# Performance work log

Measured on AMD Instinct MI355X. Metric: run time of the kernel, lower is better.

## Reference

```python
import jax, jax.numpy as jnp
import numpy as np

B, S, D = 1, 4096, 1024
H, W = 16, 512            # heads, window_size
HD = D // H               # head_dim = 64


def setup_inputs() -> dict:
    key = jax.random.key(0)
    k1, k2, k3 = jax.random.split(key, 3)
    x = jax.random.normal(k1, (B, S, D), dtype=jnp.float32)
    w_qkv = jax.random.normal(k2, (D, 3 * D), dtype=jnp.float32) * 0.02
    w_out = jax.random.normal(k3, (D, D), dtype=jnp.float32) * 0.02
    return {"x": x, "w_qkv": w_qkv, "w_out": w_out}


def reference(x, w_qkv, w_out):
    b, s, d = x.shape
    qkv = x @ w_qkv                                   # [B,S,3D]
    q, k, v = jnp.split(qkv, 3, axis=-1)
    to_heads = lambda t: t.reshape(b, s, H, HD).transpose(0, 2, 1, 3)  # [B,H,S,hd]
    q, k, v = map(to_heads, (q, k, v))

    C = s // W                                        # number of chunks
    qc = q.reshape(b, H, C, W, HD)                    # [B,H,C,W,hd]
    kc = k.reshape(b, H, C, W, HD)
    vc = v.reshape(b, H, C, W, HD)

    # each chunk attends to [previous chunk, current chunk] of K/V (2W keys)
    zero = jnp.zeros_like(kc[:, :, :1])
    k_prev = jnp.concatenate([zero, kc[:, :, :-1]], axis=2)
    v_prev = jnp.concatenate([jnp.zeros_like(vc[:, :, :1]), vc[:, :, :-1]], axis=2)
    kcat = jnp.concatenate([k_prev, kc], axis=3)      # [B,H,C,2W,hd]
    vcat = jnp.concatenate([v_prev, vc], axis=3)

    scores = jnp.einsum('bhcqd,bhckd->bhcqk', qc, kcat) / (HD ** 0.5)

    # mask: causal (abs q_pos >= abs k_pos) and k_pos >= 0 (first chunk has no prev)
    wq = jnp.arange(W)
    jk = jnp.arange(2 * W)
    ci = jnp.arange(C)
    causal = (wq[:, None] + W) >= jk[None, :]                    # [W,2W]
    valid = (ci[:, None, None] * W + jk[None, None, :] - W) >= 0  # [C,1,2W]
    mask = causal[None] & valid                                   # [C,W,2W]

    scores = jnp.where(mask[None, None], scores, -jnp.inf)
    attn = jax.nn.softmax(scores, axis=-1)
    out = jnp.einsum('bhcqk,bhckd->bhcqd', attn, vcat)            # [B,H,C,W,hd]
    out = out.reshape(b, H, s, HD).transpose(0, 2, 1, 3).reshape(b, s, d)
    return out @ w_out
```

## Files before the change

### kernel.cpp

```cpp
#include <hip/hip_runtime.h>

typedef __attribute__((ext_vector_type(8))) short short8;
typedef __attribute__((ext_vector_type(4))) float f32x4;
typedef unsigned short u16;

__device__ __forceinline__ u16 f2bf(float f) {
  unsigned int u = __float_as_uint(f);
  u += 0x7fffu + ((u >> 16) & 1u);
  return (u16)(u >> 16);
}

__device__ __forceinline__ void gld16(const void* g, void* l) {
  __builtin_amdgcn_global_load_lds((const __attribute__((address_space(1))) void*)g,
                                   (__attribute__((address_space(3))) void*)l, 16, 0, 0);
}

__global__ __launch_bounds__(256) void cast_f32_to_bf16(const float* __restrict__ in,
                                                        u16* __restrict__ out, int n8) {
  int i = blockIdx.x * 256 + threadIdx.x;
  if (i >= n8) return;
  const f32x4* p = (const f32x4*)in;
  f32x4 a = p[i * 2];
  f32x4 b = p[i * 2 + 1];
  short8 o;
#pragma unroll
  for (int j = 0; j < 4; ++j) o[j] = (short)f2bf(a[j]);
#pragma unroll
  for (int j = 0; j < 4; ++j) o[4 + j] = (short)f2bf(b[j]);
  ((short8*)out)[i] = o;
}

__global__ __launch_bounds__(256) void transpose_cast(const float* __restrict__ w,
                                                      u16* __restrict__ wT, int K, int N) {
  __shared__ float tile[32][33];
  int n0 = blockIdx.x * 32, k0 = blockIdx.y * 32;
  int r = threadIdx.x >> 5;
  int c = threadIdx.x & 31;
#pragma unroll
  for (int i = 0; i < 4; ++i)
    tile[r + i * 8][c] = w[(size_t)(k0 + r + i * 8) * N + n0 + c];
  __syncthreads();
#pragma unroll
  for (int i = 0; i < 4; ++i)
    wT[(size_t)(n0 + r + i * 8) * K + k0 + c] = f2bf(tile[c][r + i * 8]);
}

template <int MODE>
__global__ __launch_bounds__(256) void gemm_bf16(
    const u16* __restrict__ A, const u16* __restrict__ Bt, float* __restrict__ C,
    u16* __restrict__ q_out, u16* __restrict__ k_out, u16* __restrict__ v_out,
    int M, int N, int K) {
  __shared__ __align__(16) u16 As[128][64];
  __shared__ __align__(16) u16 Bs[128][64];
  const int t = threadIdx.x;
  const int lane = t & 63;
  const int wid = t >> 6;
  const int wm = wid >> 1, wn = wid & 1;
  const int l15 = lane & 15, lhi = lane >> 4;

  const int nbx = gridDim.x;
  const int bid = blockIdx.y * nbx + blockIdx.x;
  const int cpx = (nbx * gridDim.y) >> 3;
  const int wg = (bid & 7) * cpx + (bid >> 3);
  const int m0 = (wg / nbx) * 128;
  const int n0 = (wg % nbx) * 128;

  const int srow = lane >> 3;
  const int scol = (lane & 7) * 8;

  f32x4 acc[4][4];
#pragma unroll
  for (int mi = 0; mi < 4; ++mi)
#pragma unroll
    for (int ni = 0; ni < 4; ++ni) acc[mi][ni] = (f32x4){0.f, 0.f, 0.f, 0.f};

  for (int k0 = 0; k0 < K; k0 += 64) {
    __syncthreads();
#pragma unroll
    for (int i = 0; i < 4; ++i) {
      int cch = wid * 4 + i;
      int row = cch * 8 + srow;
      gld16(&A[(size_t)(m0 + row) * K + k0 + scol], &As[cch * 8][0]);
      gld16(&Bt[(size_t)(n0 + row) * K + k0 + scol], &Bs[cch * 8][0]);
    }
    __syncthreads();
#pragma unroll
    for (int kc = 0; kc < 2; ++kc) {
      short8 af[4], bf[4];
#pragma unroll
      for (int mi = 0; mi < 4; ++mi)
        af[mi] = *(const short8*)&As[wm * 64 + mi * 16 + l15][kc * 32 + lhi * 8];
#pragma unroll
      for (int ni = 0; ni < 4; ++ni)
        bf[ni] = *(const short8*)&Bs[wn * 64 + ni * 16 + l15][kc * 32 + lhi * 8];
#pragma unroll
      for (int mi = 0; mi < 4; ++mi)
#pragma unroll
        for (int ni = 0; ni < 4; ++ni)
          acc[mi][ni] = __builtin_amdgcn_mfma_f32_16x16x32_bf16(af[mi], bf[ni], acc[mi][ni], 0, 0, 0);
    }
  }

#pragma unroll
  for (int mi = 0; mi < 4; ++mi)
#pragma unroll
    for (int ni = 0; ni < 4; ++ni)
#pragma unroll
      for (int r = 0; r < 4; ++r) {
        int row = m0 + wm * 64 + mi * 16 + lhi * 4 + r;
        int col = n0 + wn * 64 + ni * 16 + l15;
        float val = acc[mi][ni][r];
        if (MODE == 0) {
          C[(size_t)row * N + col] = val;
        } else {
          int which = col >> 10;
          int d = col & 1023;
          int hh = d >> 6, hd = d & 63;
          u16* dst = (which == 0) ? q_out : ((which == 1) ? k_out : v_out);
          dst[((size_t)hh * 4096 + row) * 64 + hd] = f2bf(val);
        }
      }
}

__global__ __launch_bounds__(256) void attn_kernel(
    const u16* __restrict__ qh,
    const u16* __restrict__ kh,
    const u16* __restrict__ vh,
    u16* __restrict__ out) {
  __shared__ __align__(16) u16 Ks[2][64][64];
  __shared__ __align__(16) u16 Vt[2][66][64];
  __shared__ __align__(16) u16 Pl[4][32][72];

  const int t = threadIdx.x;
  const int lane = t & 63;
  const int w = t >> 6;
  const int l15 = lane & 15;
  const int lhi = lane >> 4;

  const int bid = blockIdx.x;
  const int wk = (bid & 7) * 64 + (bid >> 3);
  const int qt = wk & 3, c = (wk >> 2) & 7, h = wk >> 5;

  const long head_base = (long)h * 4096 * 64;
  const int q0 = qt * 128;
  const long q_gbase = head_base + (long)(c * 512 + q0) * 64;

  short8 qf[2][2];
#pragma unroll
  for (int mi = 0; mi < 2; ++mi)
#pragma unroll
    for (int kc = 0; kc < 2; ++kc)
      qf[mi][kc] = *(const short8*)&qh[q_gbase + (long)(w * 32 + mi * 16 + l15) * 64 + kc * 32 + lhi * 8];

  if (t < 128) Vt[t >> 6][64][t & 63] = 0x3F80;

  float m_run[8];
  f32x4 acc_o[2][4], acc_l[2];
#pragma unroll
  for (int i = 0; i < 8; ++i) m_run[i] = -1e30f;
#pragma unroll
  for (int mi = 0; mi < 2; ++mi) {
    acc_l[mi] = (f32x4){0.f, 0.f, 0.f, 0.f};
#pragma unroll
    for (int ni = 0; ni < 4; ++ni) acc_o[mi][ni] = (f32x4){0.f, 0.f, 0.f, 0.f};
  }

  const int kt_start = (c == 0) ? 8 : 0;
  const int kt_end = 2 * qt + 9;
  const long kv_base = head_base + ((long)c - 1) * 512 * 64;

  const int ksrow = lane >> 3;
  const int kscol = ((lane & 7) ^ (lane >> 3)) * 8;
  const int vr = t >> 3, vg = t & 7;

  {
    const int j0 = kt_start * 64;
#pragma unroll
    for (int i = 0; i < 2; ++i) {
      int cch = w * 2 + i;
      gld16(&kh[kv_base + (long)(j0 + cch * 8 + ksrow) * 64 + kscol], &Ks[0][cch * 8][0]);
    }
#pragma unroll
    for (int i = 0; i < 2; ++i) {
      int r = vr + i * 32;
      short8 vv = *(const short8*)&vh[kv_base + (long)(j0 + r) * 64 + vg * 8];
#pragma unroll
      for (int j = 0; j < 8; ++j) Vt[0][vg * 8 + j][r ^ ((vg ^ j) << 3)] = (u16)vv[j];
    }
  }
  __syncthreads();

  int cur = 0;
  for (int kt = kt_start; kt <= kt_end; ++kt) {
    const int j0 = kt * 64;
    const int nxt = cur ^ 1;
    const bool has_next = (kt < kt_end);

    short8 vpre[2];
    if (has_next) {
      const int j0n = j0 + 64;
#pragma unroll
      for (int i = 0; i < 2; ++i) {
        int cch = w * 2 + i;
        gld16(&kh[kv_base + (long)(j0n + cch * 8 + ksrow) * 64 + kscol], &Ks[nxt][cch * 8][0]);
      }
#pragma unroll
      for (int i = 0; i < 2; ++i)
        vpre[i] = *(const short8*)&vh[kv_base + (long)(j0n + vr + i * 32) * 64 + vg * 8];
    }

    const bool active = (j0 <= q0 + w * 32 + 31 + 512);
    if (active) {
      f32x4 sa[2][4];
#pragma unroll
      for (int mi = 0; mi < 2; ++mi)
#pragma unroll
        for (int ni = 0; ni < 4; ++ni) sa[mi][ni] = (f32x4){0.f, 0.f, 0.f, 0.f};
#pragma unroll
      for (int kc = 0; kc < 2; ++kc) {
        short8 kf[4];
#pragma unroll
        for (int ni = 0; ni < 4; ++ni) {
          int row = ni * 16 + l15;
          int colu = (kc * 4 + lhi) ^ (row & 7);
          kf[ni] = *(const short8*)&Ks[cur][row][colu * 8];
        }
#pragma unroll
        for (int mi = 0; mi < 2; ++mi)
#pragma unroll
          for (int ni = 0; ni < 4; ++ni)
            sa[mi][ni] = __builtin_amdgcn_mfma_f32_16x16x32_bf16(qf[mi][kc], kf[ni], sa[mi][ni], 0, 0, 0);
      }

      const float SC = 0.18033688011112042f;
      const int qrow0 = q0 + w * 32 + lhi * 4;
      const bool need_mask = (j0 + 63 > q0 + w * 32 + 512);
      float tmax[8];
#pragma unroll
      for (int i = 0; i < 8; ++i) tmax[i] = -1e30f;
      if (need_mask) {
#pragma unroll
        for (int mi = 0; mi < 2; ++mi)
#pragma unroll
          for (int ni = 0; ni < 4; ++ni) {
            int jj = j0 + ni * 16 + l15;
#pragma unroll
            for (int r = 0; r < 4; ++r) {
              float sv = sa[mi][ni][r] * SC;
              sv = (qrow0 + mi * 16 + r + 512 >= jj) ? sv : -1e30f;
              sa[mi][ni][r] = sv;
              tmax[mi * 4 + r] = fmaxf(tmax[mi * 4 + r], sv);
            }
          }
      } else {
#pragma unroll
        for (int mi = 0; mi < 2; ++mi)
#pragma unroll
          for (int ni = 0; ni < 4; ++ni)
#pragma unroll
            for (int r = 0; r < 4; ++r) {
              float sv = sa[mi][ni][r] * SC;
              sa[mi][ni][r] = sv;
              tmax[mi * 4 + r] = fmaxf(tmax[mi * 4 + r], sv);
            }
      }
#pragma unroll
      for (int i = 0; i < 8; ++i)
#pragma unroll
        for (int d = 1; d < 16; d <<= 1)
          tmax[i] = fmaxf(tmax[i], __shfl_xor(tmax[i], d, 64));

      float corr[8];
#pragma unroll
      for (int i = 0; i < 8; ++i) {
        float mn = fmaxf(m_run[i], tmax[i]);
        corr[i] = __builtin_amdgcn_exp2f(m_run[i] - mn);
        m_run[i] = mn;
      }
#pragma unroll
      for (int mi = 0; mi < 2; ++mi)
#pragma unroll
        for (int ni = 0; ni < 4; ++ni)
#pragma unroll
          for (int r = 0; r < 4; ++r) {
            float p = __builtin_amdgcn_exp2f(sa[mi][ni][r] - m_run[mi * 4 + r]);
            Pl[w][mi * 16 + lhi * 4 + r][ni * 16 + l15] = f2bf(p);
          }
#pragma unroll
      for (int mi = 0; mi < 2; ++mi) {
#pragma unroll
        for (int r = 0; r < 4; ++r) acc_l[mi][r] *= corr[mi * 4 + r];
#pragma unroll
        for (int ni = 0; ni < 4; ++ni)
#pragma unroll
          for (int r = 0; r < 4; ++r) acc_o[mi][ni][r] *= corr[mi * 4 + r];
      }
    }

    if (has_next) {
#pragma unroll
      for (int i = 0; i < 2; ++i) {
        int r = vr + i * 32;
#pragma unroll
        for (int j = 0; j < 8; ++j) Vt[nxt][vg * 8 + j][r ^ ((vg ^ j) << 3)] = (u16)vpre[i][j];
      }
    }

    if (active) {
#pragma unroll
      for (int k2 = 0; k2 < 2; ++k2) {
        short8 pf[2];
#pragma unroll
        for (int mi = 0; mi < 2; ++mi)
          pf[mi] = *(const short8*)&Pl[w][mi * 16 + l15][k2 * 32 + lhi * 8];
        short8 vones = *(const short8*)&Vt[cur][64][k2 * 32 + lhi * 8];
#pragma unroll
        for (int mi = 0; mi < 2; ++mi)
          acc_l[mi] = __builtin_amdgcn_mfma_f32_16x16x32_bf16(pf[mi], vones, acc_l[mi], 0, 0, 0);
#pragma unroll
        for (int ni = 0; ni < 4; ++ni) {
          int row = ni * 16 + l15;
          int S = ((row >> 3) ^ row) & 7;
          short8 vf = *(const short8*)&Vt[cur][row][(k2 * 32 + lhi * 8) ^ (S << 3)];
#pragma unroll
          for (int mi = 0; mi < 2; ++mi)
            acc_o[mi][ni] = __builtin_amdgcn_mfma_f32_16x16x32_bf16(pf[mi], vf, acc_o[mi][ni], 0, 0, 0);
        }
      }
    }
    __syncthreads();
    cur = nxt;
  }

#pragma unroll
  for (int mi = 0; mi < 2; ++mi)
#pragma unroll
    for (int ni = 0; ni < 4; ++ni)
#pragma unroll
      for (int r = 0; r < 4; ++r) {
        int qq = q0 + w * 32 + mi * 16 + lhi * 4 + r;
        long s = (long)c * 512 + qq;
        int col = h * 64 + ni * 16 + l15;
        float o = acc_o[mi][ni][r] / acc_l[mi][r];
        out[s * 1024 + col] = f2bf(o);
      }
}

extern "C" void kernel_launch(void* const* d_in, const int* in_sizes, int n_in,
                              void* d_out, int out_size, void* d_ws, size_t ws_size,
                              hipStream_t stream) {
  const float* x = (const float*)d_in[0];
  const float* w_qkv = (const float*)d_in[1];
  const float* w_out = (const float*)d_in[2];
  float* out = (float*)d_out;

  u16* xb = (u16*)d_ws;
  u16* wqkvT = xb + 4096 * 1024;
  u16* woutT = wqkvT + 3072 * 1024;
  u16* qh = woutT + 1024 * 1024;
  u16* kh = qh + 16 * 4096 * 64;
  u16* vh = kh + 16 * 4096 * 64;
  u16* attn = xb;

  cast_f32_to_bf16<<<2048, 256, 0, stream>>>(x, xb, 4096 * 1024 / 8);
  transpose_cast<<<dim3(96, 32), 256, 0, stream>>>(w_qkv, wqkvT, 1024, 3072);
  transpose_cast<<<dim3(32, 32), 256, 0, stream>>>(w_out, woutT, 1024, 1024);

  gemm_bf16<1><<<dim3(24, 32), 256, 0, stream>>>(xb, wqkvT, nullptr, qh, kh, vh,
                                                 4096, 3072, 1024);
  attn_kernel<<<512, 256, 0, stream>>>(qh, kh, vh, attn);
  gemm_bf16<0><<<dim3(8, 32), 256, 0, stream>>>(attn, woutT, out, nullptr, nullptr, nullptr,
                                                4096, 1024, 1024);
}
```

Baseline: 213.7 us.

## Halve attention query tile per block and add MFMA priority hints

The attention kernel now handles 64 query rows per block, 16 per wave, instead of 128 rows, which doubles the grid to 1024 blocks and cuts per-thread accumulator registers. The aim is more parallelism and occupancy across the CUs, plus less causal-tail imbalance between blocks. Each K/V tile is now loaded from global memory and staged in LDS by twice as many blocks, which raises memory traffic and makes each MFMA load do less work. s_setprio is also raised around the MFMA sections so that wave's matrix work is scheduled ahead of other waves.

```diff
diff --git a/kernel.cpp b/kernel.cpp
--- a/kernel.cpp
+++ b/kernel.cpp
@@ -129,7 +129,7 @@
     u16* __restrict__ out) {
   __shared__ __align__(16) u16 Ks[2][64][64];
   __shared__ __align__(16) u16 Vt[2][66][64];
-  __shared__ __align__(16) u16 Pl[4][32][72];
+  __shared__ __align__(16) u16 Pl[4][16][72];
 
   const int t = threadIdx.x;
   const int lane = t & 63;
@@ -138,35 +138,30 @@
   const int lhi = lane >> 4;
 
   const int bid = blockIdx.x;
-  const int wk = (bid & 7) * 64 + (bid >> 3);
-  const int qt = wk & 3, c = (wk >> 2) & 7, h = wk >> 5;
+  const int wk = (bid & 7) * 128 + (bid >> 3);
+  const int qt = wk & 7, c = (wk >> 3) & 7, h = wk >> 6;
 
   const long head_base = (long)h * 4096 * 64;
-  const int q0 = qt * 128;
+  const int q0 = qt * 64;
   const long q_gbase = head_base + (long)(c * 512 + q0) * 64;
 
-  short8 qf[2][2];
-#pragma unroll
-  for (int mi = 0; mi < 2; ++mi)
-#pragma unroll
-    for (int kc = 0; kc < 2; ++kc)
-      qf[mi][kc] = *(const short8*)&qh[q_gbase + (long)(w * 32 + mi * 16 + l15) * 64 + kc * 32 + lhi * 8];
+  short8 qf[2];
+#pragma unroll
+  for (int kc = 0; kc < 2; ++kc)
+    qf[kc] = *(const short8*)&qh[q_gbase + (long)(w * 16 + l15) * 64 + kc * 32 + lhi * 8];
 
   if (t < 128) Vt[t >> 6][64][t & 63] = 0x3F80;
 
-  float m_run[8];
-  f32x4 acc_o[2][4], acc_l[2];
-#pragma unroll
-  for (int i = 0; i < 8; ++i) m_run[i] = -1e30f;
-#pragma unroll
-  for (int mi = 0; mi < 2; ++mi) {
-    acc_l[mi] = (f32x4){0.f, 0.f, 0.f, 0.f};
-#pragma unroll
-    for (int ni = 0; ni < 4; ++ni) acc_o[mi][ni] = (f32x4){0.f, 0.f, 0.f, 0.f};
-  }
+  float m_run[4];
+  f32x4 acc_o[4], acc_l;
+#pragma unroll
+  for (int i = 0; i < 4; ++i) m_run[i] = -1e30f;
+  acc_l = (f32x4){0.f, 0.f, 0.f, 0.f};
+#pragma unroll
+  for (int ni = 0; ni < 4; ++ni) acc_o[ni] = (f32x4){0.f, 0.f, 0.f, 0.f};
 
   const int kt_start = (c == 0) ? 8 : 0;
-  const int kt_end = 2 * qt + 9;
+  const int kt_end = qt + 8;
   const long kv_base = head_base + ((long)c - 1) * 512 * 64;
 
   const int ksrow = lane >> 3;
@@ -209,13 +204,12 @@
         vpre[i] = *(const short8*)&vh[kv_base + (long)(j0n + vr + i * 32) * 64 + vg * 8];
     }
 
-    const bool active = (j0 <= q0 + w * 32 + 31 + 512);
+    const bool active = (j0 <= q0 + w * 16 + 15 + 512);
     if (active) {
-      f32x4 sa[2][4];
-#pragma unroll
-      for (int mi = 0; mi < 2; ++mi)
-#pragma unroll
-        for (int ni = 0; ni < 4; ++ni) sa[mi][ni] = (f32x4){0.f, 0.f, 0.f, 0.f};
+      f32x4 sa[4];
+#pragma unroll
+      for (int ni = 0; ni < 4; ++ni) sa[ni] = (f32x4){0.f, 0.f, 0.f, 0.f};
+      __builtin_amdgcn_s_setprio(1);
 #pragma unroll
       for (int kc = 0; kc < 2; ++kc) {
         short8 kf[4];
@@ -226,75 +220,65 @@
           kf[ni] = *(const short8*)&Ks[cur][row][colu * 8];
         }
 #pragma unroll
-        for (int mi = 0; mi < 2; ++mi)
-#pragma unroll
-          for (int ni = 0; ni < 4; ++ni)
-            sa[mi][ni] = __builtin_amdgcn_mfma_f32_16x16x32_bf16(qf[mi][kc], kf[ni], sa[mi][ni], 0, 0, 0);
-      }
+        for (int ni = 0; ni < 4; ++ni)
+          sa[ni] = __builtin_amdgcn_mfma_f32_16x16x32_bf16(qf[kc], kf[ni], sa[ni], 0, 0, 0);
+      }
+      __builtin_amdgcn_s_setprio(0);
 
       const float SC = 0.18033688011112042f;
-      const int qrow0 = q0 + w * 32 + lhi * 4;
-      const bool need_mask = (j0 + 63 > q0 + w * 32 + 512);
-      float tmax[8];
-#pragma unroll
-      for (int i = 0; i < 8; ++i) tmax[i] = -1e30f;
+      const int qrow0 = q0 + w * 16 + lhi * 4;
+      const bool need_mask = (j0 + 63 > q0 + w * 16 + 512);
+      float tmax[4];
+#pragma unroll
+      for (int i = 0; i < 4; ++i) tmax[i] = -1e30f;
       if (need_mask) {
 #pragma unroll
-        for (int mi = 0; mi < 2; ++mi)
-#pragma unroll
-          for (int ni = 0; ni < 4; ++ni) {
-            int jj = j0 + ni * 16 + l15;
-#pragma unroll
-            for (int r = 0; r < 4; ++r) {
-              float sv = sa[mi][ni][r] * SC;
-              sv = (qrow0 + mi * 16 + r + 512 >= jj) ? sv : -1e30f;
-              sa[mi][ni][r] = sv;
-              tmax[mi * 4 + r] = fmaxf(tmax[mi * 4 + r], sv);
-            }
+        for (int ni = 0; ni < 4; ++ni) {
+          int jj = j0 + ni * 16 + l15;
+#pragma unroll
+          for (int r = 0; r < 4; ++r) {
+            float sv = sa[ni][r] * SC;
+            sv = (qrow0 + r + 512 >= jj) ? sv : -1e30f;
+            sa[ni][r] = sv;
+            tmax[r] = fmaxf(tmax[r], sv);
           }
+        }
       } else {
 #pragma unroll
-        for (int mi = 0; mi < 2; ++mi)
-#pragma unroll
-          for (int ni = 0; ni < 4; ++ni)
-#pragma unroll
-            for (int r = 0; r < 4; ++r) {
-              float sv = sa[mi][ni][r] * SC;
-              sa[mi][ni][r] = sv;
-              tmax[mi * 4 + r] = fmaxf(tmax[mi * 4 + r], sv);
-            }
-      }
-#pragma unroll
-      for (int i = 0; i < 8; ++i)
+        for (int ni = 0; ni < 4; ++ni)
+#pragma unroll
+          for (int r = 0; r < 4; ++r) {
+            float sv = sa[ni][r] * SC;
+            sa[ni][r] = sv;
+            tmax[r] = fmaxf(tmax[r], sv);
+          }
+      }
+#pragma unroll
+      for (int i = 0; i < 4; ++i)
 #pragma unroll
         for (int d = 1; d < 16; d <<= 1)
           tmax[i] = fmaxf(tmax[i], __shfl_xor(tmax[i], d, 64));
 
-      float corr[8];
-#pragma unroll
-      for (int i = 0; i < 8; ++i) {
+      float corr[4];
+#pragma unroll
+      for (int i = 0; i < 4; ++i) {
         float mn = fmaxf(m_run[i], tmax[i]);
         corr[i] = __builtin_amdgcn_exp2f(m_run[i] - mn);
         m_run[i] = mn;
       }
 #pragma unroll
-      for (int mi = 0; mi < 2; ++mi)
-#pragma unroll
-        for (int ni = 0; ni < 4; ++ni)
-#pragma unroll
-          for (int r = 0; r < 4; ++r) {
-            float p = __builtin_amdgcn_exp2f(sa[mi][ni][r] - m_run[mi * 4 + r]);
-            Pl[w][mi * 16 + lhi * 4 + r][ni * 16 + l15] = f2bf(p);
-          }
-#pragma unroll
-      for (int mi = 0; mi < 2; ++mi) {
-#pragma unroll
-        for (int r = 0; r < 4; ++r) acc_l[mi][r] *= corr[mi * 4 + r];
-#pragma unroll
-        for (int ni = 0; ni < 4; ++ni)
-#pragma unroll
-          for (int r = 0; r < 4; ++r) acc_o[mi][ni][r] *= corr[mi * 4 + r];
-      }
+      for (int ni = 0; ni < 4; ++ni)
+#pragma unroll
+        for (int r = 0; r < 4; ++r) {
+          float p = __builtin_amdgcn_exp2f(sa[ni][r] - m_run[r]);
+          Pl[w][lhi * 4 + r][ni * 16 + l15] = f2bf(p);
+        }
+#pragma unroll
+      for (int r = 0; r < 4; ++r) acc_l[r] *= corr[r];
+#pragma unroll
+      for (int ni = 0; ni < 4; ++ni)
+#pragma unroll
+        for (int r = 0; r < 4; ++r) acc_o[ni][r] *= corr[r];
     }
 
     if (has_next) {
@@ -307,43 +291,36 @@
     }
 
     if (active) {
+      __builtin_amdgcn_s_setprio(1);
 #pragma unroll
       for (int k2 = 0; k2 < 2; ++k2) {
-        short8 pf[2];
-#pragma unroll
-        for (int mi = 0; mi < 2; ++mi)
-          pf[mi] = *(const short8*)&Pl[w][mi * 16 + l15][k2 * 32 + lhi * 8];
+        short8 pf = *(const short8*)&Pl[w][l15][k2 * 32 + lhi * 8];
         short8 vones = *(const short8*)&Vt[cur][64][k2 * 32 + lhi * 8];
-#pragma unroll
-        for (int mi = 0; mi < 2; ++mi)
-          acc_l[mi] = __builtin_amdgcn_mfma_f32_16x16x32_bf16(pf[mi], vones, acc_l[mi], 0, 0, 0);
+        acc_l = __builtin_amdgcn_mfma_f32_16x16x32_bf16(pf, vones, acc_l, 0, 0, 0);
 #pragma unroll
         for (int ni = 0; ni < 4; ++ni) {
           int row = ni * 16 + l15;
           int S = ((row >> 3) ^ row) & 7;
           short8 vf = *(const short8*)&Vt[cur][row][(k2 * 32 + lhi * 8) ^ (S << 3)];
-#pragma unroll
-          for (int mi = 0; mi < 2; ++mi)
-            acc_o[mi][ni] = __builtin_amdgcn_mfma_f32_16x16x32_bf16(pf[mi], vf, acc_o[mi][ni], 0, 0, 0);
-        }
-      }
+          acc_o[ni] = __builtin_amdgcn_mfma_f32_16x16x32_bf16(pf, vf, acc_o[ni], 0, 0, 0);
+        }
+      }
+      __builtin_amdgcn_s_setprio(0);
     }
     __syncthreads();
     cur = nxt;
   }
 
 #pragma unroll
-  for (int mi = 0; mi < 2; ++mi)
-#pragma unroll
-    for (int ni = 0; ni < 4; ++ni)
-#pragma unroll
-      for (int r = 0; r < 4; ++r) {
-        int qq = q0 + w * 32 + mi * 16 + lhi * 4 + r;
-        long s = (long)c * 512 + qq;
-        int col = h * 64 + ni * 16 + l15;
-        float o = acc_o[mi][ni][r] / acc_l[mi][r];
-        out[s * 1024 + col] = f2bf(o);
-      }
+  for (int ni = 0; ni < 4; ++ni)
+#pragma unroll
+    for (int r = 0; r < 4; ++r) {
+      int qq = q0 + w * 16 + lhi * 4 + r;
+      long s = (long)c * 512 + qq;
+      int col = h * 64 + ni * 16 + l15;
+      float o = acc_o[ni][r] / acc_l[r];
+      out[s * 1024 + col] = f2bf(o);
+    }
 }
 
 extern "C" void kernel_launch(void* const* d_in, const int* in_sizes, int n_in,
@@ -368,7 +345,7 @@
 
   gemm_bf16<1><<<dim3(24, 32), 256, 0, stream>>>(xb, wqkvT, nullptr, qh, kh, vh,
                                                  4096, 3072, 1024);
-  attn_kernel<<<512, 256, 0, stream>>>(qh, kh, vh, attn);
+  attn_kernel<<<1024, 256, 0, stream>>>(qh, kh, vh, attn);
   gemm_bf16<0><<<dim3(8, 32), 256, 0, stream>>>(attn, woutT, out, nullptr, nullptr, nullptr,
                                                 4096, 1024, 1024);
 }
```

After: 219.0 us. +2.4%, slower.

## Pre-transpose V, head-major attention output, swizzled GEMM LDS, fold Q scale

Applied to the files above, without the earlier changes.

Adds a separate kernel that transposes V per head. The attention kernel can then fill its V tile with direct global-to-LDS loads instead of transposing through registers and doing scattered LDS stores. Attention output is written head-major in place over the Q buffer, and the output GEMM gains a mode that reads this layout, with a narrower N tile (BN=64) to launch more blocks. The GEMM's LDS tiles are now XOR-swizzled to cut bank conflicts. The softmax scale is folded into Q in the QKV GEMM epilogue, which removes a multiply per score in attention. The cost is one extra kernel launch and an extra pass over V in memory.

```diff
diff --git a/kernel.cpp b/kernel.cpp
--- a/kernel.cpp
+++ b/kernel.cpp
@@ -45,13 +45,30 @@
     wT[(size_t)(n0 + r + i * 8) * K + k0 + c] = f2bf(tile[c][r + i * 8]);
 }
 
-template <int MODE>
+__global__ __launch_bounds__(256) void transpose_v(const u16* __restrict__ vh,
+                                                   u16* __restrict__ vt) {
+  __shared__ u16 tile[32][33];
+  const int s0 = blockIdx.x * 32, d0 = blockIdx.y * 32, h = blockIdx.z;
+  const long hb = (long)h * 4096 * 64;
+  const long hb2 = (long)h * 64 * 4096;
+  const int r = threadIdx.x >> 5, c = threadIdx.x & 31;
+#pragma unroll
+  for (int i = 0; i < 4; ++i)
+    tile[r + i * 8][c] = vh[hb + (long)(s0 + r + i * 8) * 64 + d0 + c];
+  __syncthreads();
+#pragma unroll
+  for (int i = 0; i < 4; ++i)
+    vt[hb2 + (long)(d0 + r + i * 8) * 4096 + s0 + c] = tile[c][r + i * 8];
+}
+
+template <int MODE, int BN>
 __global__ __launch_bounds__(256) void gemm_bf16(
     const u16* __restrict__ A, const u16* __restrict__ Bt, float* __restrict__ C,
     u16* __restrict__ q_out, u16* __restrict__ k_out, u16* __restrict__ v_out,
     int M, int N, int K) {
   __shared__ __align__(16) u16 As[128][64];
-  __shared__ __align__(16) u16 Bs[128][64];
+  __shared__ __align__(16) u16 Bs[BN][64];
+  constexpr int NW = BN / 32;
   const int t = threadIdx.x;
   const int lane = t & 63;
   const int wid = t >> 6;
@@ -63,16 +80,16 @@
   const int cpx = (nbx * gridDim.y) >> 3;
   const int wg = (bid & 7) * cpx + (bid >> 3);
   const int m0 = (wg / nbx) * 128;
-  const int n0 = (wg % nbx) * 128;
+  const int n0 = (wg % nbx) * BN;
 
   const int srow = lane >> 3;
-  const int scol = (lane & 7) * 8;
-
-  f32x4 acc[4][4];
+  const int scol = ((lane & 7) ^ (lane >> 3)) * 8;
+
+  f32x4 acc[4][NW];
 #pragma unroll
   for (int mi = 0; mi < 4; ++mi)
 #pragma unroll
-    for (int ni = 0; ni < 4; ++ni) acc[mi][ni] = (f32x4){0.f, 0.f, 0.f, 0.f};
+    for (int ni = 0; ni < NW; ++ni) acc[mi][ni] = (f32x4){0.f, 0.f, 0.f, 0.f};
 
   for (int k0 = 0; k0 < K; k0 += 64) {
     __syncthreads();
@@ -80,44 +97,58 @@
     for (int i = 0; i < 4; ++i) {
       int cch = wid * 4 + i;
       int row = cch * 8 + srow;
-      gld16(&A[(size_t)(m0 + row) * K + k0 + scol], &As[cch * 8][0]);
+      const u16* src = (MODE == 2)
+          ? &A[((size_t)(k0 >> 6) * 4096 + m0 + row) * 64 + scol]
+          : &A[(size_t)(m0 + row) * K + k0 + scol];
+      gld16(src, &As[cch * 8][0]);
+    }
+#pragma unroll
+    for (int i = 0; i < NW; ++i) {
+      int cch = wid * NW + i;
+      int row = cch * 8 + srow;
       gld16(&Bt[(size_t)(n0 + row) * K + k0 + scol], &Bs[cch * 8][0]);
     }
     __syncthreads();
 #pragma unroll
     for (int kc = 0; kc < 2; ++kc) {
-      short8 af[4], bf[4];
+      short8 af[4], bf[NW];
+#pragma unroll
+      for (int mi = 0; mi < 4; ++mi) {
+        int row = wm * 64 + mi * 16 + l15;
+        af[mi] = *(const short8*)&As[row][((kc * 4 + lhi) ^ (l15 & 7)) * 8];
+      }
+#pragma unroll
+      for (int ni = 0; ni < NW; ++ni) {
+        int row = wn * (BN / 2) + ni * 16 + l15;
+        bf[ni] = *(const short8*)&Bs[row][((kc * 4 + lhi) ^ (l15 & 7)) * 8];
+      }
 #pragma unroll
       for (int mi = 0; mi < 4; ++mi)
-        af[mi] = *(const short8*)&As[wm * 64 + mi * 16 + l15][kc * 32 + lhi * 8];
-#pragma unroll
-      for (int ni = 0; ni < 4; ++ni)
-        bf[ni] = *(const short8*)&Bs[wn * 64 + ni * 16 + l15][kc * 32 + lhi * 8];
-#pragma unroll
-      for (int mi = 0; mi < 4; ++mi)
-#pragma unroll
-        for (int ni = 0; ni < 4; ++ni)
+#pragma unroll
+        for (int ni = 0; ni < NW; ++ni)
           acc[mi][ni] = __builtin_amdgcn_mfma_f32_16x16x32_bf16(af[mi], bf[ni], acc[mi][ni], 0, 0, 0);
     }
   }
 
+  const float SCQ = 0.18033688011112042f;
 #pragma unroll
   for (int mi = 0; mi < 4; ++mi)
 #pragma unroll
-    for (int ni = 0; ni < 4; ++ni)
+    for (int ni = 0; ni < NW; ++ni)
 #pragma unroll
       for (int r = 0; r < 4; ++r) {
         int row = m0 + wm * 64 + mi * 16 + lhi * 4 + r;
-        int col = n0 + wn * 64 + ni * 16 + l15;
+        int col = n0 + wn * (BN / 2) + ni * 16 + l15;
         float val = acc[mi][ni][r];
-        if (MODE == 0) {
-          C[(size_t)row * N + col] = val;
-        } else {
+        if constexpr (MODE == 1) {
           int which = col >> 10;
           int d = col & 1023;
           int hh = d >> 6, hd = d & 63;
-          u16* dst = (which == 0) ? q_out : ((which == 1) ? k_out : v_out);
-          dst[((size_t)hh * 4096 + row) * 64 + hd] = f2bf(val);
+          if (which == 0)      q_out[((size_t)hh * 4096 + row) * 64 + hd] = f2bf(val * SCQ);
+          else if (which == 1) k_out[((size_t)hh * 4096 + row) * 64 + hd] = f2bf(val);
+          else                 v_out[((size_t)hh * 4096 + row) * 64 + hd] = f2bf(val);
+        } else {
+          C[(size_t)row * N + col] = val;
         }
       }
 }
@@ -125,10 +156,10 @@
 __global__ __launch_bounds__(256) void attn_kernel(
     const u16* __restrict__ qh,
     const u16* __restrict__ kh,
-    const u16* __restrict__ vh,
-    u16* __restrict__ out) {
+    const u16* __restrict__ vt,
+    u16* __restrict__ outh) {
   __shared__ __align__(16) u16 Ks[2][64][64];
-  __shared__ __align__(16) u16 Vt[2][66][64];
+  __shared__ __align__(16) u16 Vt[2][65][64];
   __shared__ __align__(16) u16 Pl[4][32][72];
 
   const int t = threadIdx.x;
@@ -168,24 +199,18 @@
   const int kt_start = (c == 0) ? 8 : 0;
   const int kt_end = 2 * qt + 9;
   const long kv_base = head_base + ((long)c - 1) * 512 * 64;
-
-  const int ksrow = lane >> 3;
-  const int kscol = ((lane & 7) ^ (lane >> 3)) * 8;
-  const int vr = t >> 3, vg = t & 7;
+  const long vt_hb = (long)h * 64 * 4096 + ((long)c - 1) * 512;
+
+  const int srow = lane >> 3;
+  const int sunit8 = ((lane & 7) ^ (lane >> 3)) * 8;
 
   {
     const int j0 = kt_start * 64;
 #pragma unroll
     for (int i = 0; i < 2; ++i) {
       int cch = w * 2 + i;
-      gld16(&kh[kv_base + (long)(j0 + cch * 8 + ksrow) * 64 + kscol], &Ks[0][cch * 8][0]);
-    }
-#pragma unroll
-    for (int i = 0; i < 2; ++i) {
-      int r = vr + i * 32;
-      short8 vv = *(const short8*)&vh[kv_base + (long)(j0 + r) * 64 + vg * 8];
-#pragma unroll
-      for (int j = 0; j < 8; ++j) Vt[0][vg * 8 + j][r ^ ((vg ^ j) << 3)] = (u16)vv[j];
+      gld16(&kh[kv_base + (long)(j0 + cch * 8 + srow) * 64 + sunit8], &Ks[0][cch * 8][0]);
+      gld16(&vt[vt_hb + (long)(cch * 8 + srow) * 4096 + j0 + sunit8], &Vt[0][cch * 8][0]);
     }
   }
   __syncthreads();
@@ -194,19 +219,15 @@
   for (int kt = kt_start; kt <= kt_end; ++kt) {
     const int j0 = kt * 64;
     const int nxt = cur ^ 1;
-    const bool has_next = (kt < kt_end);
-
-    short8 vpre[2];
-    if (has_next) {
+
+    if (kt < kt_end) {
       const int j0n = j0 + 64;
 #pragma unroll
       for (int i = 0; i < 2; ++i) {
         int cch = w * 2 + i;
-        gld16(&kh[kv_base + (long)(j0n + cch * 8 + ksrow) * 64 + kscol], &Ks[nxt][cch * 8][0]);
-      }
-#pragma unroll
-      for (int i = 0; i < 2; ++i)
-        vpre[i] = *(const short8*)&vh[kv_base + (long)(j0n + vr + i * 32) * 64 + vg * 8];
+        gld16(&kh[kv_base + (long)(j0n + cch * 8 + srow) * 64 + sunit8], &Ks[nxt][cch * 8][0]);
+        gld16(&vt[vt_hb + (long)(cch * 8 + srow) * 4096 + j0n + sunit8], &Vt[nxt][cch * 8][0]);
+      }
     }
 
     const bool active = (j0 <= q0 + w * 32 + 31 + 512);
@@ -222,8 +243,7 @@
 #pragma unroll
         for (int ni = 0; ni < 4; ++ni) {
           int row = ni * 16 + l15;
-          int colu = (kc * 4 + lhi) ^ (row & 7);
-          kf[ni] = *(const short8*)&Ks[cur][row][colu * 8];
+          kf[ni] = *(const short8*)&Ks[cur][row][((kc * 4 + lhi) ^ (l15 & 7)) * 8];
         }
 #pragma unroll
         for (int mi = 0; mi < 2; ++mi)
@@ -232,7 +252,6 @@
             sa[mi][ni] = __builtin_amdgcn_mfma_f32_16x16x32_bf16(qf[mi][kc], kf[ni], sa[mi][ni], 0, 0, 0);
       }
 
-      const float SC = 0.18033688011112042f;
       const int qrow0 = q0 + w * 32 + lhi * 4;
       const bool need_mask = (j0 + 63 > q0 + w * 32 + 512);
       float tmax[8];
@@ -246,7 +265,7 @@
             int jj = j0 + ni * 16 + l15;
 #pragma unroll
             for (int r = 0; r < 4; ++r) {
-              float sv = sa[mi][ni][r] * SC;
+              float sv = sa[mi][ni][r];
               sv = (qrow0 + mi * 16 + r + 512 >= jj) ? sv : -1e30f;
               sa[mi][ni][r] = sv;
               tmax[mi * 4 + r] = fmaxf(tmax[mi * 4 + r], sv);
@@ -258,11 +277,8 @@
 #pragma unroll
           for (int ni = 0; ni < 4; ++ni)
 #pragma unroll
-            for (int r = 0; r < 4; ++r) {
-              float sv = sa[mi][ni][r] * SC;
-              sa[mi][ni][r] = sv;
-              tmax[mi * 4 + r] = fmaxf(tmax[mi * 4 + r], sv);
-            }
+            for (int r = 0; r < 4; ++r)
+              tmax[mi * 4 + r] = fmaxf(tmax[mi * 4 + r], sa[mi][ni][r]);
       }
 #pragma unroll
       for (int i = 0; i < 8; ++i)
@@ -295,18 +311,7 @@
 #pragma unroll
           for (int r = 0; r < 4; ++r) acc_o[mi][ni][r] *= corr[mi * 4 + r];
       }
-    }
-
-    if (has_next) {
-#pragma unroll
-      for (int i = 0; i < 2; ++i) {
-        int r = vr + i * 32;
-#pragma unroll
-        for (int j = 0; j < 8; ++j) Vt[nxt][vg * 8 + j][r ^ ((vg ^ j) << 3)] = (u16)vpre[i][j];
-      }
-    }
-
-    if (active) {
+
 #pragma unroll
       for (int k2 = 0; k2 < 2; ++k2) {
         short8 pf[2];
@@ -320,8 +325,7 @@
 #pragma unroll
         for (int ni = 0; ni < 4; ++ni) {
           int row = ni * 16 + l15;
-          int S = ((row >> 3) ^ row) & 7;
-          short8 vf = *(const short8*)&Vt[cur][row][(k2 * 32 + lhi * 8) ^ (S << 3)];
+          short8 vf = *(const short8*)&Vt[cur][row][((k2 * 4 + lhi) ^ (l15 & 7)) * 8];
 #pragma unroll
           for (int mi = 0; mi < 2; ++mi)
             acc_o[mi][ni] = __builtin_amdgcn_mfma_f32_16x16x32_bf16(pf[mi], vf, acc_o[mi][ni], 0, 0, 0);
@@ -340,9 +344,8 @@
       for (int r = 0; r < 4; ++r) {
         int qq = q0 + w * 32 + mi * 16 + lhi * 4 + r;
         long s = (long)c * 512 + qq;
-        int col = h * 64 + ni * 16 + l15;
         float o = acc_o[mi][ni][r] / acc_l[mi][r];
-        out[s * 1024 + col] = f2bf(o);
+        outh[(head_base + s * 64) + ni * 16 + l15] = f2bf(o);
       }
 }
 
@@ -360,15 +363,16 @@
   u16* qh = woutT + 1024 * 1024;
   u16* kh = qh + 16 * 4096 * 64;
   u16* vh = kh + 16 * 4096 * 64;
-  u16* attn = xb;
+  u16* vt = xb;
 
   cast_f32_to_bf16<<<2048, 256, 0, stream>>>(x, xb, 4096 * 1024 / 8);
   transpose_cast<<<dim3(96, 32), 256, 0, stream>>>(w_qkv, wqkvT, 1024, 3072);
   transpose_cast<<<dim3(32, 32), 256, 0, stream>>>(w_out, woutT, 1024, 1024);
 
-  gemm_bf16<1><<<dim3(24, 32), 256, 0, stream>>>(xb, wqkvT, nullptr, qh, kh, vh,
-                                                 4096, 3072, 1024);
-  attn_kernel<<<512, 256, 0, stream>>>(qh, kh, vh, attn);
-  gemm_bf16<0><<<dim3(8, 32), 256, 0, stream>>>(attn, woutT, out, nullptr, nullptr, nullptr,
-                                                4096, 1024, 1024);
-}
+  gemm_bf16<1, 128><<<dim3(24, 32), 256, 0, stream>>>(xb, wqkvT, nullptr, qh, kh, vh,
+                                                      4096, 3072, 1024);
+  transpose_v<<<dim3(128, 2, 16), 256, 0, stream>>>(vh, vt);
+  attn_kernel<<<512, 256, 0, stream>>>(qh, kh, vt, qh);
+  gemm_bf16<2, 64><<<dim3(16, 32), 256, 0, stream>>>(qh, woutT, out, nullptr, nullptr, nullptr,
+                                                     4096, 1024, 1024);
+}
```

Result: faster. 187.4 us (-12.3%).
